# Kernel tuning notes

Hardware: AMD Instinct MI355X
Metric: run time of the kernel (lower is better)

Reference implementation:

```python
import jax, jax.numpy as jnp
import numpy as np

B, T, F, M = 32, 256, 512, 4   # batch, pred_len (=d_model=state_size), feature_dim (=mamba seq), time-mark feats
N = F - M                      # number of variates in x_enc
T2 = 2 * T
EPS = 1e-5


def setup_inputs() -> dict:
    key = jax.random.key(0)
    it = iter(jax.random.split(key, 32))
    def nrm(*s):
        return jax.random.normal(next(it), s, jnp.float32) * 0.02
    inp = {
        "x_enc": jax.random.normal(next(it), (B, T, N), jnp.float32),
        "x_mark_enc": jax.random.normal(next(it), (B, T, M), jnp.float32),
        "x_dec": jnp.zeros((1, 1, 1), jnp.float32),
        "x_mark_dec": jnp.zeros((1, 1, 1), jnp.float32),
        # 3 structurally identical MambaBlocks -> stack params on leading dim 3
        "norm_w": jnp.ones((3, T), jnp.float32),
        "inp_W": nrm(3, T, T2), "inp_b": jnp.zeros((3, T2), jnp.float32),
        "conv_W": nrm(3, F, F, 3), "conv_b": jnp.zeros((3, F), jnp.float32),
        "convlin_W": nrm(3, T2, T2), "convlin_b": jnp.zeros((3, T2), jnp.float32),
        "fc1_W": nrm(3, T2, T2), "fc1_b": jnp.zeros((3, T2), jnp.float32),
        "fc2_W": nrm(3, T2, T), "fc2_b": jnp.zeros((3, T), jnp.float32),
        "fc3_W": nrm(3, T2, T), "fc3_b": jnp.zeros((3, T), jnp.float32),
        "D_W": nrm(3, T, T2), "D_b": jnp.zeros((3, T2), jnp.float32),
        "out_W": nrm(3, T2, T), "out_b": jnp.ones((3, T), jnp.float32),  # out_proj.bias init to 1.0
        "proj_W": nrm(T, T), "proj_b": jnp.zeros((T,), jnp.float32),
    }
    return inp


def _rmsnorm(x, w):
    return x * jax.lax.rsqrt(jnp.mean(x * x, -1, keepdims=True) + EPS) * w


def _conv1d(x, W, b):
    # x: [B, C, L], W: [C_out, C_in, 3], padding=1
    y = jax.lax.conv_general_dilated(x, W, (1,), [(1, 1)], dimension_numbers=("NCH", "OIH", "NCH"))
    return y + b[None, :, None]


def _s6(x, fc1W, fc1b, fc2W, fc2b, fc3W, fc3b):
    # h is zero-initialized each call, so dA=exp(delta*A) multiplies zeros and
    # y = einsum('bln,bldn->bld', C, x[...,None]*dB) = delta * x * <C,B>_n
    Bmat = x @ fc2W + fc2b                         # [B, L, n]
    Cmat = x @ fc3W + fc3b                         # [B, L, n]
    delta = jax.nn.softplus(x @ fc1W + fc1b)       # [B, L, d]
    cb = jnp.einsum("bln,bln->bl", Cmat, Bmat)   # contraction over state dim
    return delta * x * cb[:, :, None]


def _block(x, i, p):
    xn = _rmsnorm(x, p["norm_w"][i])
    xp = xn @ p["inp_W"][i] + p["inp_b"][i]                      # [B, F, 2T]
    xc = jax.nn.silu(_conv1d(xp, p["conv_W"][i], p["conv_b"][i]))
    xco = xc @ p["convlin_W"][i] + p["convlin_b"][i]
    xssm = _s6(xco, p["fc1_W"][i], p["fc1_b"][i], p["fc2_W"][i], p["fc2_b"][i], p["fc3_W"][i], p["fc3_b"][i])
    xres = jax.nn.silu(xn @ p["D_W"][i] + p["D_b"][i])
    return (jax.nn.silu(xssm) * xres) @ p["out_W"][i] + p["out_b"][i]


def _forward(x_enc, x_mark_enc, p):
    means = jax.lax.stop_gradient(jnp.mean(x_enc, 1, keepdims=True))  # detached in torch
    xe = x_enc - means
    stdev = jnp.sqrt(jnp.var(xe, axis=1, keepdims=True) + 1e-5)       # NOT detached in torch
    xe = xe / stdev
    x = jnp.concatenate([xe, x_mark_enc], axis=2).transpose(0, 2, 1)  # [B, F, T]
    for i in range(3):
        x = _block(x, i, p)
    dec = (x @ p["proj_W"] + p["proj_b"]).transpose(0, 2, 1)          # [B, T, F]
    return dec[:, :, :N] * stdev + means                              # pred_len == T


def reference(x_enc, x_mark_enc, x_dec, x_mark_dec, norm_w, inp_W, inp_b, conv_W, conv_b, convlin_W, convlin_b, fc1_W, fc1_b, fc2_W, fc2_b, fc3_W, fc3_b, D_W, D_b, out_W, out_b, proj_W, proj_b):
    p = dict(norm_w=norm_w, inp_W=inp_W, inp_b=inp_b, conv_W=conv_W, conv_b=conv_b, convlin_W=convlin_W, convlin_b=convlin_b, fc1_W=fc1_W, fc1_b=fc1_b, fc2_W=fc2_W, fc2_b=fc2_b, fc3_W=fc3_W, fc3_b=fc3_b, D_W=D_W, D_b=D_b, out_W=out_W, out_b=out_b, proj_W=proj_W, proj_b=proj_b)
    return _forward(x_enc, x_mark_enc, p)
```

## Files before the change

kernel.cpp:

```cpp
#include <hip/hip_runtime.h>
#include <hip/hip_bf16.h>
#include <math.h>

typedef __hip_bfloat16 bf16;
typedef short short8 __attribute__((ext_vector_type(8)));
typedef short short4v __attribute__((ext_vector_type(4)));
typedef float floatx4 __attribute__((ext_vector_type(4)));

constexpr int CB_ = 32;
constexpr int CT = 256;
constexpr int CF = 512;
constexpr int CN = 508;
constexpr int CM = 4;
constexpr int CT2 = 512;
constexpr int MROWS = CB_ * CF;
constexpr int PADL = 528;

__device__ __forceinline__ float b2f(bf16 v) { return __bfloat162float(v); }
__device__ __forceinline__ bf16 f2b(float v) { return __float2bfloat16(v); }
__device__ __forceinline__ float silu_f(float x) { return x / (1.0f + expf(-x)); }
__device__ __forceinline__ float softplus_f(float x) {
    return fmaxf(x, 0.0f) + log1pf(expf(-fabsf(x)));
}

__device__ __forceinline__ void gl_lds16(const bf16* g, short* l) {
    __builtin_amdgcn_global_load_lds(
        (const __attribute__((address_space(1))) unsigned int*)(g),
        (__attribute__((address_space(3))) unsigned int*)(l), 16, 0, 0);
}

struct P8 { const float* s[8]; bf16* d[8]; };
__global__ __launch_bounds__(256) void prepack_all_kernel(P8 p) {
    const int Ks[8]   = {256, 256, 512, 512, 512, 512, 512, 256};
    const int Ns[8]   = {512, 512, 512, 256, 256, 512, 256, 256};
    const int zs[8]   = {3, 3, 3, 3, 3, 3, 3, 1};
    const int dstr[8] = {262144, 262144, 524288, 524288, 524288, 262144, 131072, 65536};
    int bid = blockIdx.x;
    int m = 0, acc = 0;
    for (m = 0; m < 8; m++) {
        int c = (Ns[m] >> 5) * (Ks[m] >> 5) * zs[m];
        if (bid < acc + c) break;
        acc += c;
    }
    int lid = bid - acc;
    int K = Ks[m], N = Ns[m];
    int tx = N >> 5, ty = K >> 5;
    int z = lid / (tx * ty), rem = lid % (tx * ty);
    int k0 = (rem / tx) * 32, n0 = (rem % tx) * 32;
    const float* s = p.s[m] + (size_t)z * K * N;
    bf16* d = p.d[m] + (size_t)z * dstr[m];
    __shared__ float Ts[32][33];
    for (int e = threadIdx.x; e < 1024; e += 256) {
        int r = e >> 5, c = e & 31;
        Ts[r][c] = s[(size_t)(k0 + r) * N + n0 + c];
    }
    __syncthreads();
    for (int e = threadIdx.x; e < 1024; e += 256) {
        int r = e >> 5, c = e & 31;
        d[(size_t)(n0 + r) * K + k0 + c] = f2b(Ts[c][r]);
    }
}

constexpr int CONVN = 3 * 3 * 512 * 512;
__global__ void convpack_kernel(const float* __restrict__ src, bf16* __restrict__ dst,
                                bf16* __restrict__ xpT) {
    int idx = blockIdx.x * 256 + threadIdx.x;
    if (idx < CONVN) {
        int ci = idx & 511;
        int co = (idx >> 9) & 511;
        int it = idx >> 18;
        int tap = it % 3, ib = it / 3;
        dst[idx] = f2b(src[(((size_t)(ib * 512 + co)) * 512 + ci) * 3 + tap]);
    } else if (idx < CONVN + 32768) {
        int j = idx - CONVN;
        int ci = j & 511;
        int w = (j >> 9) & 1;
        int b = j >> 10;
        xpT[((size_t)b * PADL + (w ? 513 : 0)) * 512 + ci] = f2b(0.0f);
    }
}

__global__ __launch_bounds__(256) void buildx_rms_kernel(
    const float* __restrict__ xe, const float* __restrict__ xm,
    const float* __restrict__ nw, float* __restrict__ means, float* __restrict__ stdev,
    bf16* __restrict__ XN) {
    __shared__ float rbuf[4];
    int row = blockIdx.x;
    int b = row >> 9, f = row & 511;
    int t = threadIdx.x;
    int lane = t & 63, wid = t >> 6;
    float val;
    if (f < CN) {
        float v = xe[(size_t)b * CT * CN + t * CN + f];
        float s = v;
        #pragma unroll
        for (int o = 32; o > 0; o >>= 1) s += __shfl_xor(s, o);
        if (lane == 0) rbuf[wid] = s;
        __syncthreads();
        float mean = (rbuf[0] + rbuf[1] + rbuf[2] + rbuf[3]) * (1.0f / CT);
        __syncthreads();
        float d = v - mean;
        float s2 = d * d;
        #pragma unroll
        for (int o = 32; o > 0; o >>= 1) s2 += __shfl_xor(s2, o);
        if (lane == 0) rbuf[wid] = s2;
        __syncthreads();
        float var = (rbuf[0] + rbuf[1] + rbuf[2] + rbuf[3]) * (1.0f / CT);
        __syncthreads();
        float sd = sqrtf(var + 1e-5f);
        if (t == 0) {
            means[b * CN + f] = mean;
            stdev[b * CN + f] = sd;
        }
        val = d / sd;
    } else {
        val = xm[(size_t)b * CT * CM + t * CM + (f - CN)];
    }
    float ss = val * val;
    #pragma unroll
    for (int o = 32; o > 0; o >>= 1) ss += __shfl_xor(ss, o);
    if (lane == 0) rbuf[wid] = ss;
    __syncthreads();
    float total = rbuf[0] + rbuf[1] + rbuf[2] + rbuf[3];
    float scale = rsqrtf(total * (1.0f / CT) + 1e-5f);
    XN[(size_t)row * CT + t] = f2b(val * scale * nw[t]);
}

template <int MODE>
__global__ __launch_bounds__(256) void mgemm_kernel(const bf16* __restrict__ A,
                                                    const bf16* __restrict__ Wt,
                                                    const float* __restrict__ b1,
                                                    const float* __restrict__ b2,
                                                    const float* __restrict__ b3,
                                                    bf16* __restrict__ o1,
                                                    bf16* __restrict__ o2,
                                                    int K, int Ncols) {
    __shared__ __align__(16) short As[128 * 32];
    __shared__ __align__(16) short Bs[128 * 32];
    const int tid = threadIdx.x;
    const int lane = tid & 63;
    const int wave = tid >> 6;
    const int m0 = blockIdx.x * 128, n0 = blockIdx.y * 128;

    const int srow0 = wave * 32;
    const int lrow = lane >> 2;
    const int lcol = (lane & 3) * 8;

    const bf16* aP0 = A + (size_t)(m0 + srow0 + lrow) * K + lcol;
    const bf16* aP1 = A + (size_t)(m0 + srow0 + 16 + lrow) * K + lcol;
    const bf16* bP0 = Wt + (size_t)(n0 + srow0 + lrow) * K + lcol;
    const bf16* bP1 = Wt + (size_t)(n0 + srow0 + 16 + lrow) * K + lcol;
    short* aL0 = &As[srow0 * 32];
    short* aL1 = &As[(srow0 + 16) * 32];
    short* bL0 = &Bs[srow0 * 32];
    short* bL1 = &Bs[(srow0 + 16) * 32];

    const int wm = (wave & 1) * 64, wn = (wave >> 1) * 64;
    const int fr = lane & 15, quad = lane >> 4;

    floatx4 acc[4][4];
    #pragma unroll
    for (int i = 0; i < 4; i++)
        #pragma unroll
        for (int j = 0; j < 4; j++) acc[i][j] = (floatx4){0.f, 0.f, 0.f, 0.f};

    for (int k0 = 0; k0 < K; k0 += 32) {
        gl_lds16(aP0 + k0, aL0);
        gl_lds16(aP1 + k0, aL1);
        gl_lds16(bP0 + k0, bL0);
        gl_lds16(bP1 + k0, bL1);
        __syncthreads();
        short8 af[4], bfv[4];
        #pragma unroll
        for (int i = 0; i < 4; i++) af[i] = *(const short8*)&As[(wm + i * 16 + fr) * 32 + quad * 8];
        #pragma unroll
        for (int j = 0; j < 4; j++) bfv[j] = *(const short8*)&Bs[(wn + j * 16 + fr) * 32 + quad * 8];
        #pragma unroll
        for (int i = 0; i < 4; i++)
            #pragma unroll
            for (int j = 0; j < 4; j++)
                acc[i][j] = __builtin_amdgcn_mfma_f32_16x16x32_bf16(af[i], bfv[j], acc[i][j], 0, 0, 0);
        __syncthreads();
    }

    if (MODE == 0) {
        #pragma unroll
        for (int j = 0; j < 4; j++) {
            int n = n0 + wn + j * 16 + fr;
            float bv = b1[n];
            #pragma unroll
            for (int i = 0; i < 4; i++) {
                int mb = m0 + wm + i * 16 + quad * 4;
                #pragma unroll
                for (int r = 0; r < 4; r++)
                    o1[(size_t)(mb + r) * Ncols + n] = f2b(acc[i][j][r] + bv);
            }
        }
    } else if (MODE == 1) {
        if (n0 + wn < 512) {
            int b = (m0 + wm) >> 9;
            #pragma unroll
            for (int j = 0; j < 4; j++) {
                int n = n0 + wn + j * 16 + fr;
                float bv = b1[n];
                bf16* dst = o1 + ((size_t)b * PADL + n + 1) * 512;
                #pragma unroll
                for (int i = 0; i < 4; i++) {
                    int ci = (m0 + wm + i * 16 + quad * 4) & 511;
                    short4v pk;
                    #pragma unroll
                    for (int r = 0; r < 4; r++) {
                        bf16 tb = f2b(acc[i][j][r] + bv);
                        pk[r] = __builtin_bit_cast(short, tb);
                    }
                    *(short4v*)(dst + ci) = pk;
                }
            }
        } else {
            #pragma unroll
            for (int j = 0; j < 4; j++) {
                int n = n0 + wn + j * 16 + fr;
                float bv = b2[n - 512];
                #pragma unroll
                for (int i = 0; i < 4; i++) {
                    int mb = m0 + wm + i * 16 + quad * 4;
                    #pragma unroll
                    for (int r = 0; r < 4; r++)
                        o2[(size_t)(mb + r) * 512 + (n - 512)] = f2b(silu_f(acc[i][j][r] + bv));
                }
            }
        }
    } else {
        if (n0 + wn < 512) {
            #pragma unroll
            for (int j = 0; j < 4; j++) {
                int n = n0 + wn + j * 16 + fr;
                float bv = b1[n];
                #pragma unroll
                for (int i = 0; i < 4; i++) {
                    int mb = m0 + wm + i * 16 + quad * 4;
                    #pragma unroll
                    for (int r = 0; r < 4; r++)
                        o1[(size_t)(mb + r) * 512 + n] = f2b(acc[i][j][r] + bv);
                }
            }
        } else {
            #pragma unroll
            for (int j = 0; j < 4; j++) {
                int n = n0 + wn + j * 16 + fr;
                float bv = (n < 768) ? b2[n - 512] : b3[n - 768];
                #pragma unroll
                for (int i = 0; i < 4; i++) {
                    int mb = m0 + wm + i * 16 + quad * 4;
                    #pragma unroll
                    for (int r = 0; r < 4; r++)
                        o2[(size_t)(mb + r) * 512 + (n - 512)] = f2b(acc[i][j][r] + bv);
                }
            }
        }
    }
}

__global__ __launch_bounds__(256) void conv_mfma_kernel(const bf16* __restrict__ Wc,
                                                        const bf16* __restrict__ xpT,
                                                        const float* __restrict__ bias,
                                                        bf16* __restrict__ Out) {
    __shared__ __align__(16) short As[3 * 128 * 32];
    __shared__ __align__(16) short Bs[144 * 32];
    const int tid = threadIdx.x;
    const int lane = tid & 63;
    const int wave = tid >> 6;
    int bx = blockIdx.x;
    int xcd = bx & 7, g = bx >> 3;
    int mt = g & 3;
    int id = xcd * 16 + (g >> 2);
    int nt = id & 3, b = id >> 2;
    const int m0 = mt * 128, n0 = nt * 128;
    const bf16* xb = xpT + (size_t)b * PADL * 512;

    const int lrow = lane >> 2;
    const int lcol = (lane & 3) * 8;
    const int wm = (wave & 1) * 64, wn = (wave >> 1) * 64;
    const int fr = lane & 15, quad = lane >> 4;

    floatx4 acc[4][4];
    #pragma unroll
    for (int i = 0; i < 4; i++)
        #pragma unroll
        for (int j = 0; j < 4; j++) acc[i][j] = (floatx4){0.f, 0.f, 0.f, 0.f};

    for (int k0 = 0; k0 < 512; k0 += 32) {
        for (int ga = wave; ga < 24; ga += 4) {
            int tap = ga >> 3, rg = ga & 7;
            gl_lds16(Wc + (size_t)tap * 262144 + (size_t)(m0 + rg * 16 + lrow) * 512 + k0 + lcol,
                     &As[ga * 512]);
        }
        for (int gb = wave; gb < 9; gb += 4) {
            gl_lds16(xb + (size_t)(n0 + gb * 16 + lrow) * 512 + k0 + lcol, &Bs[gb * 512]);
        }
        __syncthreads();
        #pragma unroll
        for (int tap = 0; tap < 3; tap++) {
            short8 af[4], bfv[4];
            #pragma unroll
            for (int i = 0; i < 4; i++)
                af[i] = *(const short8*)&As[tap * 4096 + (wm + i * 16 + fr) * 32 + quad * 8];
            #pragma unroll
            for (int j = 0; j < 4; j++)
                bfv[j] = *(const short8*)&Bs[(wn + j * 16 + fr + tap) * 32 + quad * 8];
            #pragma unroll
            for (int i = 0; i < 4; i++)
                #pragma unroll
                for (int j = 0; j < 4; j++)
                    acc[i][j] = __builtin_amdgcn_mfma_f32_16x16x32_bf16(af[i], bfv[j], acc[i][j], 0, 0, 0);
        }
        __syncthreads();
    }
    bf16* ob = Out + (size_t)b * CF * CT2;
    #pragma unroll
    for (int i = 0; i < 4; i++) {
        int mb = m0 + wm + i * 16 + quad * 4;
        #pragma unroll
        for (int r = 0; r < 4; r++) {
            float bv = bias[mb + r];
            #pragma unroll
            for (int j = 0; j < 4; j++) {
                int n = n0 + wn + j * 16 + fr;
                ob[(size_t)(mb + r) * CT2 + n] = f2b(silu_f(acc[i][j][r] + bv));
            }
        }
    }
}

__global__ __launch_bounds__(256) void gate_kernel(bf16* __restrict__ P,
                                                   const bf16* __restrict__ xco,
                                                   const bf16* __restrict__ E,
                                                   const bf16* __restrict__ xres) {
    __shared__ float red[4];
    int row = blockIdx.x;
    int t = threadIdx.x;
    size_t base = (size_t)row * 512;
    float s = b2f(E[base + t]) * b2f(E[base + 256 + t]);
    #pragma unroll
    for (int o = 32; o > 0; o >>= 1) s += __shfl_down(s, o);
    if ((t & 63) == 0) red[t >> 6] = s;
    __syncthreads();
    float cb = red[0] + red[1] + red[2] + red[3];
    #pragma unroll
    for (int h = 0; h < 2; h++) {
        size_t idx = base + t + h * 256;
        float delta = softplus_f(b2f(P[idx]));
        float xssm = delta * b2f(xco[idx]) * cb;
        P[idx] = f2b(silu_f(xssm) * b2f(xres[idx]));
    }
}

__global__ __launch_bounds__(256) void gemm_rms_kernel(const bf16* __restrict__ A,
                                                       const bf16* __restrict__ Wt,
                                                       const float* __restrict__ bias,
                                                       const float* __restrict__ nw,
                                                       bf16* __restrict__ Xo,
                                                       bf16* __restrict__ XNo) {
    __shared__ __align__(16) short As[64 * 32];
    __shared__ __align__(16) short Bs[256 * 32];
    __shared__ float red[4][64];
    __shared__ float scl[64];
    const int tid = threadIdx.x;
    const int lane = tid & 63;
    const int wave = tid >> 6;
    const int m0 = blockIdx.x * 64;

    const int lrow = lane >> 2;
    const int lcol = (lane & 3) * 8;
    const bf16* aP = A + (size_t)(m0 + wave * 16 + lrow) * 512 + lcol;
    short* aL = &As[wave * 16 * 32];
    const bf16* bP[4];
    short* bL[4];
    #pragma unroll
    for (int g = 0; g < 4; g++) {
        int r0 = (wave * 4 + g) * 16;
        bP[g] = Wt + (size_t)(r0 + lrow) * 512 + lcol;
        bL[g] = &Bs[r0 * 32];
    }
    const int wn = wave * 64;
    const int fr = lane & 15, quad = lane >> 4;

    floatx4 acc[4][4];
    #pragma unroll
    for (int i = 0; i < 4; i++)
        #pragma unroll
        for (int j = 0; j < 4; j++) acc[i][j] = (floatx4){0.f, 0.f, 0.f, 0.f};

    for (int k0 = 0; k0 < 512; k0 += 32) {
        gl_lds16(aP + k0, aL);
        #pragma unroll
        for (int g = 0; g < 4; g++) gl_lds16(bP[g] + k0, bL[g]);
        __syncthreads();
        short8 af[4], bfv[4];
        #pragma unroll
        for (int i = 0; i < 4; i++) af[i] = *(const short8*)&As[(i * 16 + fr) * 32 + quad * 8];
        #pragma unroll
        for (int j = 0; j < 4; j++) bfv[j] = *(const short8*)&Bs[(wn + j * 16 + fr) * 32 + quad * 8];
        #pragma unroll
        for (int i = 0; i < 4; i++)
            #pragma unroll
            for (int j = 0; j < 4; j++)
                acc[i][j] = __builtin_amdgcn_mfma_f32_16x16x32_bf16(af[i], bfv[j], acc[i][j], 0, 0, 0);
        __syncthreads();
    }
    #pragma unroll
    for (int j = 0; j < 4; j++) {
        float bv = bias[wn + j * 16 + fr];
        #pragma unroll
        for (int i = 0; i < 4; i++)
            #pragma unroll
            for (int r = 0; r < 4; r++) acc[i][j][r] += bv;
    }
    #pragma unroll
    for (int i = 0; i < 4; i++) {
        #pragma unroll
        for (int r = 0; r < 4; r++) {
            float s = 0.f;
            #pragma unroll
            for (int j = 0; j < 4; j++) s += acc[i][j][r] * acc[i][j][r];
            #pragma unroll
            for (int o = 8; o > 0; o >>= 1) s += __shfl_xor(s, o);
            if (fr == 0) red[wave][i * 16 + quad * 4 + r] = s;
        }
    }
    __syncthreads();
    if (tid < 64) {
        float tot = red[0][tid] + red[1][tid] + red[2][tid] + red[3][tid];
        scl[tid] = rsqrtf(tot * (1.0f / CT) + 1e-5f);
    }
    __syncthreads();
    #pragma unroll
    for (int j = 0; j < 4; j++) {
        int n = wn + j * 16 + fr;
        float w = nw[n];
        #pragma unroll
        for (int i = 0; i < 4; i++) {
            int rl = i * 16 + quad * 4;
            #pragma unroll
            for (int r = 0; r < 4; r++) {
                float v = acc[i][j][r];
                Xo[(size_t)(m0 + rl + r) * CT + n] = f2b(v);
                XNo[(size_t)(m0 + rl + r) * CT + n] = f2b(v * scl[rl + r] * w);
            }
        }
    }
}

__global__ __launch_bounds__(256) void proj_out_kernel(const bf16* __restrict__ A,
                                                       const bf16* __restrict__ Wt,
                                                       const float* __restrict__ bias,
                                                       const float* __restrict__ means,
                                                       const float* __restrict__ stdev,
                                                       float* __restrict__ out) {
    __shared__ __align__(16) short As[128 * 32];
    __shared__ __align__(16) short Bs[128 * 32];
    const int tid = threadIdx.x;
    const int lane = tid & 63;
    const int wave = tid >> 6;
    const int m0 = blockIdx.x * 128, n0 = blockIdx.y * 128;

    const int srow0 = wave * 32;
    const int lrow = lane >> 2;
    const int lcol = (lane & 3) * 8;
    const bf16* aP0 = A + (size_t)(m0 + srow0 + lrow) * 256 + lcol;
    const bf16* aP1 = A + (size_t)(m0 + srow0 + 16 + lrow) * 256 + lcol;
    const bf16* bP0 = Wt + (size_t)(n0 + srow0 + lrow) * 256 + lcol;
    const bf16* bP1 = Wt + (size_t)(n0 + srow0 + 16 + lrow) * 256 + lcol;
    short* aL0 = &As[srow0 * 32];
    short* aL1 = &As[(srow0 + 16) * 32];
    short* bL0 = &Bs[srow0 * 32];
    short* bL1 = &Bs[(srow0 + 16) * 32];

    const int wm = (wave & 1) * 64, wn = (wave >> 1) * 64;
    const int fr = lane & 15, quad = lane >> 4;

    floatx4 acc[4][4];
    #pragma unroll
    for (int i = 0; i < 4; i++)
        #pragma unroll
        for (int j = 0; j < 4; j++) acc[i][j] = (floatx4){0.f, 0.f, 0.f, 0.f};

    for (int k0 = 0; k0 < 256; k0 += 32) {
        gl_lds16(aP0 + k0, aL0);
        gl_lds16(aP1 + k0, aL1);
        gl_lds16(bP0 + k0, bL0);
        gl_lds16(bP1 + k0, bL1);
        __syncthreads();
        short8 af[4], bfv[4];
        #pragma unroll
        for (int i = 0; i < 4; i++) af[i] = *(const short8*)&As[(wm + i * 16 + fr) * 32 + quad * 8];
        #pragma unroll
        for (int j = 0; j < 4; j++) bfv[j] = *(const short8*)&Bs[(wn + j * 16 + fr) * 32 + quad * 8];
        #pragma unroll
        for (int i = 0; i < 4; i++)
            #pragma unroll
            for (int j = 0; j < 4; j++)
                acc[i][j] = __builtin_amdgcn_mfma_f32_16x16x32_bf16(af[i], bfv[j], acc[i][j], 0, 0, 0);
        __syncthreads();
    }
    #pragma unroll
    for (int j = 0; j < 4; j++) {
        int t = n0 + wn + j * 16 + fr;
        float bv = bias[t];
        #pragma unroll
        for (int i = 0; i < 4; i++) {
            int mb = m0 + wm + i * 16 + quad * 4;
            int b = mb >> 9;
            int nv = mb & 511;
            if (nv < CN) {
                floatx4 o;
                #pragma unroll
                for (int r = 0; r < 4; r++) {
                    int sn = b * CN + nv + r;
                    o[r] = (acc[i][j][r] + bv) * stdev[sn] + means[sn];
                }
                *(floatx4*)(out + ((size_t)(b * CT + t)) * CN + nv) = o;
            }
        }
    }
}

extern "C" void kernel_launch(void* const* d_in, const int* in_sizes, int n_in,
                              void* d_out, int out_size, void* d_ws, size_t ws_size,
                              hipStream_t stream) {
    const float* x_enc  = (const float*)d_in[0];
    const float* x_mark = (const float*)d_in[1];
    const float* norm_w = (const float*)d_in[4];
    const float* inp_W  = (const float*)d_in[5];
    const float* inp_b  = (const float*)d_in[6];
    const float* conv_W = (const float*)d_in[7];
    const float* conv_b = (const float*)d_in[8];
    const float* convlin_W = (const float*)d_in[9];
    const float* convlin_b = (const float*)d_in[10];
    const float* fc1_W = (const float*)d_in[11];
    const float* fc1_b = (const float*)d_in[12];
    const float* fc2_W = (const float*)d_in[13];
    const float* fc2_b = (const float*)d_in[14];
    const float* fc3_W = (const float*)d_in[15];
    const float* fc3_b = (const float*)d_in[16];
    const float* D_W   = (const float*)d_in[17];
    const float* D_b   = (const float*)d_in[18];
    const float* out_W = (const float*)d_in[19];
    const float* out_b = (const float*)d_in[20];
    const float* proj_W = (const float*)d_in[21];
    const float* proj_b = (const float*)d_in[22];

    char* ws = (char*)d_ws;
    float* MEANS = (float*)(ws);
    float* STDEV = (float*)(ws + 65536);
    bf16* wt = (bf16*)(ws + 131072);
    bf16* wt_g1      = wt;
    bf16* wt_g3      = wt + 786432;
    bf16* wt_convlin = wt + 2359296;
    bf16* wt_out     = wt + 3145728;
    bf16* wt_proj    = wt + 3538944;
    bf16* wt_conv    = wt + 3604480;
    bf16* xpT = (bf16*)(ws + 12058624);
    const size_t POOLB = 16777216;
    const size_t HALF = 16384 * 256;
    bf16* pool[3] = {
        (bf16*)(ws + 29360128),
        (bf16*)(ws + 29360128 + POOLB),
        (bf16*)(ws + 29360128 + 2 * POOLB),
    };
    bf16* E = (bf16*)(ws + 29360128 + 3 * POOLB);
    float* out = (float*)d_out;

    P8 p;
    p.s[0] = inp_W;  p.d[0] = wt_g1;
    p.s[1] = D_W;    p.d[1] = wt_g1 + 131072;
    p.s[2] = fc1_W;  p.d[2] = wt_g3;
    p.s[3] = fc2_W;  p.d[3] = wt_g3 + 262144;
    p.s[4] = fc3_W;  p.d[4] = wt_g3 + 393216;
    p.s[5] = convlin_W; p.d[5] = wt_convlin;
    p.s[6] = out_W;  p.d[6] = wt_out;
    p.s[7] = proj_W; p.d[7] = wt_proj;
    prepack_all_kernel<<<3520, 256, 0, stream>>>(p);
    convpack_kernel<<<(CONVN + 32768 + 255) / 256, 256, 0, stream>>>(conv_W, wt_conv, xpT);

    buildx_rms_kernel<<<MROWS, 256, 0, stream>>>(x_enc, x_mark, norm_w, MEANS, STDEV,
                                                 pool[0] + HALF);

    for (int i = 0; i < 3; i++) {
        bf16* A  = pool[i % 3];
        bf16* Bp = pool[(i + 1) % 3];
        bf16* Cp = pool[(i + 2) % 3];
        bf16* XN = A + HALF;

        mgemm_kernel<1><<<dim3(128, 8), 256, 0, stream>>>(
            XN, wt_g1 + (size_t)i * 262144, inp_b + i * CT2, D_b + i * CT2, nullptr,
            xpT, Cp, 256, 1024);
        conv_mfma_kernel<<<512, 256, 0, stream>>>(wt_conv + (size_t)i * 786432, xpT,
                                                  conv_b + i * CF, A);
        mgemm_kernel<0><<<dim3(128, 4), 256, 0, stream>>>(
            A, wt_convlin + (size_t)i * 262144, convlin_b + i * CT2, nullptr, nullptr,
            Bp, nullptr, 512, 512);
        mgemm_kernel<3><<<dim3(128, 8), 256, 0, stream>>>(
            Bp, wt_g3 + (size_t)i * 524288, fc1_b + i * CT2, fc2_b + i * CT, fc3_b + i * CT,
            A, E, 512, 1024);
        gate_kernel<<<MROWS, 256, 0, stream>>>(A, Bp, E, Cp);
        gemm_rms_kernel<<<256, 256, 0, stream>>>(
            A, wt_out + (size_t)i * 131072, out_b + i * CT,
            norm_w + ((i + 1) % 3) * CT, Bp, Bp + HALF);
    }

    proj_out_kernel<<<dim3(128, 2), 256, 0, stream>>>(
        pool[0], wt_proj, proj_b, MEANS, STDEV, out);
}
```

Baseline: 641.0 us.

## Tile input normalization over feature blocks and halve conv N-tile for more blocks

```diff
diff --git a/kernel.cpp b/kernel.cpp
--- a/kernel.cpp
+++ b/kernel.cpp
@@ -84,46 +84,59 @@
     const float* __restrict__ xe, const float* __restrict__ xm,
     const float* __restrict__ nw, float* __restrict__ means, float* __restrict__ stdev,
     bf16* __restrict__ XN) {
-    __shared__ float rbuf[4];
-    int row = blockIdx.x;
-    int b = row >> 9, f = row & 511;
-    int t = threadIdx.x;
-    int lane = t & 63, wid = t >> 6;
-    float val;
-    if (f < CN) {
-        float v = xe[(size_t)b * CT * CN + t * CN + f];
-        float s = v;
-        #pragma unroll
-        for (int o = 32; o > 0; o >>= 1) s += __shfl_xor(s, o);
-        if (lane == 0) rbuf[wid] = s;
-        __syncthreads();
-        float mean = (rbuf[0] + rbuf[1] + rbuf[2] + rbuf[3]) * (1.0f / CT);
-        __syncthreads();
-        float d = v - mean;
-        float s2 = d * d;
-        #pragma unroll
-        for (int o = 32; o > 0; o >>= 1) s2 += __shfl_xor(s2, o);
-        if (lane == 0) rbuf[wid] = s2;
-        __syncthreads();
-        float var = (rbuf[0] + rbuf[1] + rbuf[2] + rbuf[3]) * (1.0f / CT);
-        __syncthreads();
-        float sd = sqrtf(var + 1e-5f);
-        if (t == 0) {
-            means[b * CN + f] = mean;
-            stdev[b * CN + f] = sd;
-        }
-        val = d / sd;
-    } else {
-        val = xm[(size_t)b * CT * CM + t * CM + (f - CN)];
-    }
-    float ss = val * val;
-    #pragma unroll
-    for (int o = 32; o > 0; o >>= 1) ss += __shfl_xor(ss, o);
-    if (lane == 0) rbuf[wid] = ss;
+    __shared__ float L[256][65];
+    __shared__ float red_s[4][64], red_q[4][64];
+    __shared__ float stat_m[64], stat_i[64], scl[64];
+    int blk = blockIdx.x;
+    int b = blk >> 3, f0 = (blk & 7) * 64;
+    int tid = threadIdx.x;
+    int j = tid & 63, tq = tid >> 6;
+    int f = f0 + j;
+    float ps = 0.f, pq = 0.f;
+    const float* xep = xe + (size_t)b * CT * CN + f;
+    const float* xmp = xm + (size_t)b * CT * CM + (f - CN);
+    #pragma unroll 4
+    for (int tt = 0; tt < 64; tt++) {
+        int t = tq * 64 + tt;
+        float v = (f < CN) ? xep[(size_t)t * CN] : xmp[(size_t)t * CM];
+        L[t][j] = v;
+        ps += v;
+        pq += v * v;
+    }
+    red_s[tq][j] = ps;
+    red_q[tq][j] = pq;
     __syncthreads();
-    float total = rbuf[0] + rbuf[1] + rbuf[2] + rbuf[3];
-    float scale = rsqrtf(total * (1.0f / CT) + 1e-5f);
-    XN[(size_t)row * CT + t] = f2b(val * scale * nw[t]);
+    if (tid < 64) {
+        int ff = f0 + tid;
+        float s = red_s[0][tid] + red_s[1][tid] + red_s[2][tid] + red_s[3][tid];
+        float q = red_q[0][tid] + red_q[1][tid] + red_q[2][tid] + red_q[3][tid];
+        float mean, isd, msq;
+        if (ff < CN) {
+            mean = s * (1.0f / 256.0f);
+            float var = fmaxf(q * (1.0f / 256.0f) - mean * mean, 0.0f);
+            float sd = sqrtf(var + 1e-5f);
+            isd = 1.0f / sd;
+            means[b * CN + ff] = mean;
+            stdev[b * CN + ff] = sd;
+            msq = var / (var + 1e-5f);
+        } else {
+            mean = 0.0f;
+            isd = 1.0f;
+            msq = q * (1.0f / 256.0f);
+        }
+        stat_m[tid] = mean;
+        stat_i[tid] = isd;
+        scl[tid] = rsqrtf(msq + 1e-5f);
+    }
+    __syncthreads();
+    bf16* outp = XN + ((size_t)(b * 512 + f0)) * 256;
+    int t = tid;
+    float w = nw[t];
+    #pragma unroll 4
+    for (int fp = 0; fp < 64; fp++) {
+        float val = (L[t][fp] - stat_m[fp]) * stat_i[fp];
+        outp[(size_t)fp * 256 + t] = f2b(val * scl[fp] * w);
+    }
 }
 
 template <int MODE>
@@ -266,52 +279,67 @@
                                                         const float* __restrict__ bias,
                                                         bf16* __restrict__ Out) {
     __shared__ __align__(16) short As[3 * 128 * 32];
-    __shared__ __align__(16) short Bs[144 * 32];
+    __shared__ __align__(16) short Bs[80 * 32];
     const int tid = threadIdx.x;
     const int lane = tid & 63;
     const int wave = tid >> 6;
     int bx = blockIdx.x;
     int xcd = bx & 7, g = bx >> 3;
     int mt = g & 3;
-    int id = xcd * 16 + (g >> 2);
-    int nt = id & 3, b = id >> 2;
-    const int m0 = mt * 128, n0 = nt * 128;
+    int nt = (g >> 2) & 7;
+    int b = xcd * 4 + (g >> 5);
+    const int m0 = mt * 128, n0 = nt * 64;
     const bf16* xb = xpT + (size_t)b * PADL * 512;
 
     const int lrow = lane >> 2;
     const int lcol = (lane & 3) * 8;
-    const int wm = (wave & 1) * 64, wn = (wave >> 1) * 64;
+    const int wm = (wave & 1) * 64, wn = (wave >> 1) * 32;
     const int fr = lane & 15, quad = lane >> 4;
 
-    floatx4 acc[4][4];
+    const bf16* aPtr[6];
+    short* aLds[6];
+    #pragma unroll
+    for (int u = 0; u < 6; u++) {
+        int ga = wave + 4 * u;
+        int tap = ga >> 3, rg = ga & 7;
+        aPtr[u] = Wc + (size_t)tap * 262144 + (size_t)(m0 + rg * 16 + lrow) * 512 + lcol;
+        aLds[u] = &As[ga * 512];
+    }
+    const bf16* bPtr0 = xb + (size_t)(n0 + wave * 16 + lrow) * 512 + lcol;
+    short* bLds0 = &Bs[wave * 16 * 32];
+    const bf16* bPtr1 = xb + (size_t)(n0 + 64 + lrow) * 512 + lcol;
+    short* bLds1 = &Bs[64 * 32];
+
+    floatx4 acc[4][2];
     #pragma unroll
     for (int i = 0; i < 4; i++)
         #pragma unroll
-        for (int j = 0; j < 4; j++) acc[i][j] = (floatx4){0.f, 0.f, 0.f, 0.f};
+        for (int j = 0; j < 2; j++) acc[i][j] = (floatx4){0.f, 0.f, 0.f, 0.f};
 
     for (int k0 = 0; k0 < 512; k0 += 32) {
-        for (int ga = wave; ga < 24; ga += 4) {
-            int tap = ga >> 3, rg = ga & 7;
-            gl_lds16(Wc + (size_t)tap * 262144 + (size_t)(m0 + rg * 16 + lrow) * 512 + k0 + lcol,
-                     &As[ga * 512]);
-        }
-        for (int gb = wave; gb < 9; gb += 4) {
-            gl_lds16(xb + (size_t)(n0 + gb * 16 + lrow) * 512 + k0 + lcol, &Bs[gb * 512]);
-        }
+        #pragma unroll
+        for (int u = 0; u < 6; u++) {
+            gl_lds16(aPtr[u], aLds[u]);
+            aPtr[u] += 32;
+        }
+        gl_lds16(bPtr0, bLds0);
+        bPtr0 += 32;
+        if (wave == 0) gl_lds16(bPtr1, bLds1);
+        bPtr1 += 32;
         __syncthreads();
         #pragma unroll
         for (int tap = 0; tap < 3; tap++) {
-            short8 af[4], bfv[4];
+            short8 af[4], bfv[2];
             #pragma unroll
             for (int i = 0; i < 4; i++)
                 af[i] = *(const short8*)&As[tap * 4096 + (wm + i * 16 + fr) * 32 + quad * 8];
             #pragma unroll
-            for (int j = 0; j < 4; j++)
+            for (int j = 0; j < 2; j++)
                 bfv[j] = *(const short8*)&Bs[(wn + j * 16 + fr + tap) * 32 + quad * 8];
             #pragma unroll
             for (int i = 0; i < 4; i++)
                 #pragma unroll
-                for (int j = 0; j < 4; j++)
+                for (int j = 0; j < 2; j++)
                     acc[i][j] = __builtin_amdgcn_mfma_f32_16x16x32_bf16(af[i], bfv[j], acc[i][j], 0, 0, 0);
         }
         __syncthreads();
@@ -324,7 +352,7 @@
         for (int r = 0; r < 4; r++) {
             float bv = bias[mb + r];
             #pragma unroll
-            for (int j = 0; j < 4; j++) {
+            for (int j = 0; j < 2; j++) {
                 int n = n0 + wn + j * 16 + fr;
                 ob[(size_t)(mb + r) * CT2 + n] = f2b(silu_f(acc[i][j][r] + bv));
             }
@@ -583,8 +611,8 @@
     prepack_all_kernel<<<3520, 256, 0, stream>>>(p);
     convpack_kernel<<<(CONVN + 32768 + 255) / 256, 256, 0, stream>>>(conv_W, wt_conv, xpT);
 
-    buildx_rms_kernel<<<MROWS, 256, 0, stream>>>(x_enc, x_mark, norm_w, MEANS, STDEV,
-                                                 pool[0] + HALF);
+    buildx_rms_kernel<<<256, 256, 0, stream>>>(x_enc, x_mark, norm_w, MEANS, STDEV,
+                                               pool[0] + HALF);
 
     for (int i = 0; i < 3; i++) {
         bf16* A  = pool[i % 3];
@@ -595,8 +623,8 @@
         mgemm_kernel<1><<<dim3(128, 8), 256, 0, stream>>>(
             XN, wt_g1 + (size_t)i * 262144, inp_b + i * CT2, D_b + i * CT2, nullptr,
             xpT, Cp, 256, 1024);
-        conv_mfma_kernel<<<512, 256, 0, stream>>>(wt_conv + (size_t)i * 786432, xpT,
-                                                  conv_b + i * CF, A);
+        conv_mfma_kernel<<<1024, 256, 0, stream>>>(wt_conv + (size_t)i * 786432, xpT,
+                                                   conv_b + i * CF, A);
         mgemm_kernel<0><<<dim3(128, 4), 256, 0, stream>>>(
             A, wt_convlin + (size_t)i * 262144, convlin_b + i * CT2, nullptr, nullptr,
             Bp, nullptr, 512, 512);
```

Result: slower. 671.0 us (+4.7%).
